# Optimization experiments

Hardware: AMD Instinct MI355X
Metric: run time of the kernel (lower is better)

Reference implementation:

```python
import jax, jax.numpy as jnp
import numpy as np

B_, T_, N_, C_ = 8, 24, 207, 128      # batch, time (fixed 24), nodes (fixed 207), channels
RED = C_ // 2                          # reducted_size = 64 (Mamba d_model)
DIN = 2 * RED                          # Mamba d_inner (expand=2) = 128
DS, DCONV, DTR = 16, 4, 4              # d_state, d_conv, dt_rank = ceil(64/16)


def _ln(x, w, b, eps=1e-5):
    m = jnp.mean(x, -1, keepdims=True)
    v = jnp.mean((x - m) ** 2, -1, keepdims=True)
    return (x - m) * jax.lax.rsqrt(v + eps) * w + b


def _causal_conv(x, w, b):
    # depthwise causal conv along seq; x: (B,L,D), w: (D,K)
    K = w.shape[1]
    L = x.shape[1]
    xp = jnp.pad(x, ((0, 0), (K - 1, 0), (0, 0)))
    return sum(xp[:, k:k + L, :] * w[:, k] for k in range(K)) + b


def _mamba(h, inproj, conv_w, conv_b, xproj, dtw, dtb, Alog, Dp, outproj):
    # mamba_ssm Mamba(d_model=RED) forward, eval mode
    xz = h @ inproj                                        # (B,L,2*DIN)
    u, z = jnp.split(xz, 2, axis=-1)
    u = jax.nn.silu(_causal_conv(u, conv_w, conv_b))       # (B,L,DIN)
    xdbl = u @ xproj                                       # (B,L,DTR+2*DS)
    dt = jax.nn.softplus(xdbl[..., :DTR] @ dtw + dtb)      # (B,L,DIN)
    Bm = xdbl[..., DTR:DTR + DS]                           # (B,L,DS)
    Cm = xdbl[..., DTR + DS:]                              # (B,L,DS)
    A = -jnp.exp(Alog)                                     # (DIN,DS)

    def step(hs, inp):
        dt_t, B_t, C_t, u_t = inp                          # (B,DIN),(B,DS),(B,DS),(B,DIN)
        hs = hs * jnp.exp(dt_t[..., None] * A) + (dt_t * u_t)[..., None] * B_t[:, None, :]
        return hs, jnp.einsum('bdn,bn->bd', hs, C_t)

    h0 = jnp.zeros((u.shape[0], DIN, DS), u.dtype)
    xs = (dt.swapaxes(0, 1), Bm.swapaxes(0, 1), Cm.swapaxes(0, 1), u.swapaxes(0, 1))
    _, ys = jax.lax.scan(step, h0, xs)                     # (L,B,DIN)
    y = ys.swapaxes(0, 1) + u * Dp
    y = y * jax.nn.silu(z)
    return y @ outproj                                     # (B,L,RED)


def setup_inputs() -> dict:
    key = jax.random.key(0)
    ks = iter(jax.random.split(key, 64))

    def rn(shape, s):
        return jax.random.normal(next(ks), shape, jnp.float32) * s

    inp = {
        "x": jax.random.normal(next(ks), (B_, T_, N_, C_), jnp.float32),
        "qk": jax.random.normal(next(ks), (B_, T_, N_, C_), jnp.float32),
        "in_ln_w": jnp.ones(2 * C_), "in_ln_b": jnp.zeros(2 * C_),
        "in_w": rn((2 * C_, RED), 0.05), "in_b": jnp.zeros(RED),
        "ov_ln_w": jnp.ones(RED), "ov_ln_b": jnp.zeros(RED),
        "ov_w": rn((RED, C_), 0.05), "ov_b": jnp.zeros(C_),
        "o_ln_w": jnp.ones(C_), "o_ln_b": jnp.zeros(C_),
        "o_w": rn((C_, C_), 0.05), "o_b": jnp.zeros(C_),
    }
    for p in ("fw", "bw"):
        inp[p + "_inproj"] = rn((RED, 2 * DIN), 0.05)
        inp[p + "_conv_w"] = rn((DIN, DCONV), 0.2)
        inp[p + "_conv_b"] = jnp.zeros(DIN)
        inp[p + "_xproj"] = rn((DIN, DTR + 2 * DS), 0.05)
        inp[p + "_dtw"] = rn((DTR, DIN), 0.2)
        dt0 = jnp.exp(jax.random.uniform(next(ks), (DIN,)) * (np.log(0.1) - np.log(1e-3)) + np.log(1e-3))
        inp[p + "_dtb"] = jnp.log(jnp.expm1(dt0))          # inverse softplus (mamba dt init)
        inp[p + "_Alog"] = jnp.log(jnp.broadcast_to(jnp.arange(1, DS + 1, dtype=jnp.float32), (DIN, DS)))
        inp[p + "_D"] = jnp.ones(DIN)
        inp[p + "_outproj"] = rn((DIN, RED), 0.05)
    return inp


def reference(x, qk, in_ln_w, in_ln_b, in_w, in_b,
              fw_inproj, fw_conv_w, fw_conv_b, fw_xproj, fw_dtw, fw_dtb, fw_Alog, fw_D, fw_outproj,
              bw_inproj, bw_conv_w, bw_conv_b, bw_xproj, bw_dtw, bw_dtb, bw_Alog, bw_D, bw_outproj,
              ov_ln_w, ov_ln_b, ov_w, ov_b, o_ln_w, o_ln_b, o_w, o_b):
    x_in = x
    h = jnp.concatenate([x, qk], -1).reshape(B_ * T_, N_, 2 * C_)   # 'b t n f -> (b t) n f'
    h = _ln(h, in_ln_w, in_ln_b) @ in_w + in_b                       # (B*T, N, RED)
    h_fw = _mamba(h, fw_inproj, fw_conv_w, fw_conv_b, fw_xproj, fw_dtw, fw_dtb, fw_Alog, fw_D, fw_outproj)
    h_bw = _mamba(h[:, ::-1], bw_inproj, bw_conv_w, bw_conv_b, bw_xproj, bw_dtw, bw_dtb, bw_Alog, bw_D, bw_outproj)[:, ::-1]
    h = h_fw + h_bw
    h = _ln(h, ov_ln_w, ov_ln_b) @ ov_w + ov_b                       # dropout: eval no-op
    h = h.reshape(B_, T_, N_, C_) + x_in                             # '(b t) n f -> b t n f' + residual
    return _ln(h, o_ln_w, o_ln_b) @ o_w + o_b
```

## Files before the change

### kernel.cpp

```cpp
#include <hip/hip_runtime.h>
#include <hip/hip_bf16.h>

#define B__ 8
#define T__ 24
#define N__ 207
#define C__ 128
#define BT_ 192
#define L__ 207
#define RED_ 64
#define DIN_ 128
#define DS_ 16
#define DTR_ 4
#define XD_ 36
#define NC_ 6
#define CHK_ 35
#define NROW_ 39744

#define P_OVLNW 0
#define P_OVLNB 64
#define P_OVB   128
#define P_OLNW  256
#define P_OLNB  384
#define P_OB    512
#define P_INB   640
#define P_LNW   704
#define P_LNB   960
#define P_TOT   1216

using bf16 = __hip_bfloat16;

typedef __attribute__((ext_vector_type(8))) short bf8v;
typedef __attribute__((ext_vector_type(4))) short s4v;
typedef __attribute__((ext_vector_type(4))) float f4v;

__device__ __forceinline__ float ldin(const void* __restrict__ p, int i, int md) {
    if (md) return ((const float*)p)[i];
    return __bfloat162float(((const bf16*)p)[i]);
}
__device__ __forceinline__ float ldbf(const bf16* __restrict__ p, int i) {
    return __bfloat162float(p[i]);
}

__device__ __forceinline__ short f2bf(float f) {
    unsigned u = __builtin_bit_cast(unsigned, f);
    unsigned r = (u + 0x7FFFu + ((u >> 16) & 1u)) >> 16;
    return (short)(unsigned short)r;
}
__device__ __forceinline__ float bfl(short h) {
    return __builtin_bit_cast(float, ((unsigned)(unsigned short)h) << 16);
}

__global__ void k0_detect(const void* __restrict__ lnw, int* __restrict__ mode,
                          int* __restrict__ geo) {
    unsigned short h0 = ((const unsigned short*)lnw)[0];
    *mode = (h0 == 0x3F80u) ? 0 : 1;
    *geo  = 1;
}

__global__ void probe_order_dict() {}
__global__ void probe_order_signature() {}

__global__ __launch_bounds__(256) void k_prep(
    const void* __restrict__ op_fw, const void* __restrict__ op_bw,
    const void* __restrict__ ovw, const void* __restrict__ ow,
    const void* __restrict__ ovlnw, const void* __restrict__ ovlnb,
    const void* __restrict__ ovb,
    const void* __restrict__ olnw, const void* __restrict__ olnb,
    const void* __restrict__ ob,
    const void* __restrict__ inw, const void* __restrict__ inb,
    const void* __restrict__ inlnw, const void* __restrict__ inlnb,
    const void* __restrict__ ipj_fw, const void* __restrict__ ipj_bw,
    const void* __restrict__ cw_fw, const void* __restrict__ cb_fw,
    const void* __restrict__ cw_bw, const void* __restrict__ cb_bw,
    const void* __restrict__ xp_fw, const void* __restrict__ xp_bw,
    const void* __restrict__ Alog_fw, const void* __restrict__ Alog_bw,
    short* __restrict__ w0t_hi, short* __restrict__ w0t_lo,
    short* __restrict__ w2t_hi, short* __restrict__ w2t_lo,
    short* __restrict__ w1t_hi, short* __restrict__ w1t_lo,
    short* __restrict__ ovwt_hi, short* __restrict__ ovwt_lo,
    short* __restrict__ owt_hi, short* __restrict__ owt_lo,
    short* __restrict__ w3t_hi, short* __restrict__ w3t_lo,
    float* __restrict__ cwt, float* __restrict__ cbt,
    float* __restrict__ pars, const int* __restrict__ mode,
    int* __restrict__ geo)
{
    const int md = *mode;
    const int stride = gridDim.x * blockDim.x;
    const int t0 = blockIdx.x * blockDim.x + threadIdx.x;
    for (int i = t0; i < 64*256; i += stride) {
        int c = i >> 8, k = i & 255;
        float wv = ldin(inw, k*64 + c, md);
        short h = f2bf(wv); w0t_hi[i] = h; w0t_lo[i] = f2bf(wv - bfl(h));
    }
    for (int i = t0; i < 2*256*64; i += stride) {
        int dir = i >> 14, c = (i >> 6) & 255, k = i & 63;
        const void* src = dir ? ipj_bw : ipj_fw;
        float wv = ldin(src, k*256 + c, md);
        short h = f2bf(wv); w2t_hi[i] = h; w2t_lo[i] = f2bf(wv - bfl(h));
    }
    for (int i = t0; i < 64*256; i += stride) {
        int c = i >> 8, k = i & 255;
        float wv = (k < 128) ? ldin(op_fw, k*64 + c, md)
                             : ldin(op_bw, (k-128)*64 + c, md);
        short h = f2bf(wv); w1t_hi[i] = h; w1t_lo[i] = f2bf(wv - bfl(h));
    }
    for (int i = t0; i < 128*64; i += stride) {
        int c = i >> 6, k = i & 63;
        float wv = ldin(ovw, k*128 + c, md);
        short h = f2bf(wv); ovwt_hi[i] = h; ovwt_lo[i] = f2bf(wv - bfl(h));
    }
    for (int i = t0; i < 128*128; i += stride) {
        int c = i >> 7, k = i & 127;
        float wv = ldin(ow, k*128 + c, md);
        short h = f2bf(wv); owt_hi[i] = h; owt_lo[i] = f2bf(wv - bfl(h));
    }
    for (int i = t0; i < 2*48*128; i += stride) {
        int dir = i / 6144, rem = i % 6144;
        int c = rem >> 7, k = rem & 127;
        float wv = (c < XD_) ? ldin(dir ? xp_bw : xp_fw, k*XD_ + c, md) : 0.f;
        short h = f2bf(wv); w3t_hi[i] = h; w3t_lo[i] = f2bf(wv - bfl(h));
    }
    for (int i = t0; i < 2*4*128; i += stride) {
        int dir = i >> 9, k = (i >> 7) & 3, d = i & 127;
        cwt[i] = ldin(dir ? cw_bw : cw_fw, d*4 + k, md);
    }
    for (int i = t0; i < 2*128; i += stride) {
        int dir = i >> 7, d = i & 127;
        cbt[i] = ldin(dir ? cb_bw : cb_fw, d, md);
    }
    for (int i = t0; i < 2*DIN_*DS_; i += stride) {
        int dir = i >> 11, rem = i & 2047;
        int d = rem >> 4, s = rem & 15;
        const void* Al = dir ? Alog_bw : Alog_fw;
        float A  = -__expf(ldin(Al, d*DS_ + s, md));
        float A0 = -__expf(ldin(Al, d*DS_ + 0, md));
        float tgt = (float)(s + 1) * A0;
        float tol = 1e-4f * fabsf(tgt) + 1e-6f;
        if (fabsf(A - tgt) > tol) atomicAnd(geo, 0);
    }
    for (int i = t0; i < P_TOT; i += stride) {
        float v;
        if      (i < 64)   v = ldin(ovlnw, i,        md);
        else if (i < 128)  v = ldin(ovlnb, i-64,     md);
        else if (i < 256)  v = ldin(ovb,   i-128,    md);
        else if (i < 384)  v = ldin(olnw,  i-256,    md);
        else if (i < 512)  v = ldin(olnb,  i-384,    md);
        else if (i < 640)  v = ldin(ob,    i-512,    md);
        else if (i < 704)  v = ldin(inb,   i-640,    md);
        else if (i < 960)  v = ldin(inlnw, i-704,    md);
        else               v = ldin(inlnb, i-960,    md);
        pars[i] = v;
    }
}

__global__ __launch_bounds__(64) void k12_mfma(
    const void* __restrict__ x, const void* __restrict__ qk,
    const short* __restrict__ w0t_hi, const short* __restrict__ w0t_lo,
    const short* __restrict__ w2t_hi, const short* __restrict__ w2t_lo,
    const float* __restrict__ pars,
    bf16* __restrict__ uraw, bf16* __restrict__ zbuf,
    const int* __restrict__ mode)
{
    const int md  = *mode;
    const int l   = threadIdx.x;
    const int lg  = l >> 4;
    const int lc  = l & 15;
    const int wrow = blockIdx.x * 16;
    const int dir  = blockIdx.y >> 1;
    const int nh   = blockIdx.y & 1;
    const int r = wrow + lc;

    __shared__ __align__(16) short t0h[16][136];
    __shared__ __align__(16) short t0l[16][136];
    __shared__ __align__(16) short hlds[16][80];

    const f4v zero = {0.f, 0.f, 0.f, 0.f};

    float s = 0.f, ss = 0.f;
    if (md) {
        const float* sp = ((lg < 2) ? (const float*)x : (const float*)qk)
                          + (size_t)r * C__ + (lg & 1) * 64;
#pragma unroll
        for (int t = 0; t < 16; ++t) {
            float4 v = *reinterpret_cast<const float4*>(sp + 4*t);
            s  += v.x + v.y + v.z + v.w;
            ss += v.x*v.x + v.y*v.y + v.z*v.z + v.w*v.w;
        }
    } else {
        const short* sp = ((lg < 2) ? (const short*)x : (const short*)qk)
                          + (size_t)r * C__ + (lg & 1) * 64;
#pragma unroll
        for (int t = 0; t < 8; ++t) {
            bf8v v = *reinterpret_cast<const bf8v*>(sp + 8*t);
#pragma unroll
            for (int e = 0; e < 8; ++e) { float f = bfl(v[e]); s += f; ss += f*f; }
        }
    }
    s  += __shfl_xor(s, 16, 64);  ss += __shfl_xor(ss, 16, 64);
    s  += __shfl_xor(s, 32, 64);  ss += __shfl_xor(ss, 32, 64);
    const float mean = s * (1.f/256.f);
    const float rs   = rsqrtf(ss * (1.f/256.f) - mean*mean + 1e-5f);

    f4v acc1[4];
#pragma unroll
    for (int nt = 0; nt < 4; ++nt) acc1[nt] = zero;

#pragma unroll
    for (int p = 0; p < 2; ++p) {
        const int hb = lg * 32;
        const int gcb = p * 128 + hb;
        if (md) {
            const float* sp = (p ? (const float*)qk : (const float*)x)
                              + (size_t)r * C__ + hb;
#pragma unroll
            for (int t = 0; t < 8; ++t) {
                float4 v = *reinterpret_cast<const float4*>(sp + 4*t);
                float vv[4] = {v.x, v.y, v.z, v.w};
                s4v hi, lo;
#pragma unroll
                for (int e = 0; e < 4; ++e) {
                    int gc = gcb + 4*t + e;
                    float a = (vv[e] - mean) * rs * pars[P_LNW + gc] + pars[P_LNB + gc];
                    short h = f2bf(a); hi[e] = h; lo[e] = f2bf(a - bfl(h));
                }
                *reinterpret_cast<s4v*>(&t0h[lc][hb + 4*t]) = hi;
                *reinterpret_cast<s4v*>(&t0l[lc][hb + 4*t]) = lo;
            }
        } else {
            const short* sp = (p ? (const short*)qk : (const short*)x)
                              + (size_t)r * C__ + hb;
#pragma unroll
            for (int t = 0; t < 4; ++t) {
                bf8v v = *reinterpret_cast<const bf8v*>(sp + 8*t);
#pragma unroll
                for (int hh = 0; hh < 2; ++hh) {
                    s4v hi, lo;
#pragma unroll
                    for (int e = 0; e < 4; ++e) {
                        int gc = gcb + 8*t + 4*hh + e;
                        float a = (bfl(v[4*hh+e]) - mean) * rs * pars[P_LNW + gc] + pars[P_LNB + gc];
                        short h = f2bf(a); hi[e] = h; lo[e] = f2bf(a - bfl(h));
                    }
                    *reinterpret_cast<s4v*>(&t0h[lc][hb + 8*t + 4*hh]) = hi;
                    *reinterpret_cast<s4v*>(&t0l[lc][hb + 8*t + 4*hh]) = lo;
                }
            }
        }
        __syncthreads();
#pragma unroll
        for (int kk = 0; kk < 4; ++kk) {
            bf8v ah = *reinterpret_cast<const bf8v*>(&t0h[lc][kk*32 + lg*8]);
            bf8v al = *reinterpret_cast<const bf8v*>(&t0l[lc][kk*32 + lg*8]);
#pragma unroll
            for (int nt = 0; nt < 4; ++nt) {
                const int bo = (nt*16 + lc)*256 + p*128 + kk*32 + lg*8;
                bf8v bh = *reinterpret_cast<const bf8v*>(w0t_hi + bo);
                bf8v bl = *reinterpret_cast<const bf8v*>(w0t_lo + bo);
                acc1[nt] = __builtin_amdgcn_mfma_f32_16x16x32_bf16(ah, bl, acc1[nt], 0, 0, 0);
                acc1[nt] = __builtin_amdgcn_mfma_f32_16x16x32_bf16(al, bh, acc1[nt], 0, 0, 0);
                acc1[nt] = __builtin_amdgcn_mfma_f32_16x16x32_bf16(ah, bh, acc1[nt], 0, 0, 0);
            }
        }
        __syncthreads();
    }

#pragma unroll
    for (int nt = 0; nt < 4; ++nt)
#pragma unroll
        for (int j = 0; j < 4; ++j)
            hlds[lg*4 + j][nt*16 + lc] = f2bf(acc1[nt][j] + pars[P_INB + nt*16 + lc]);
    __syncthreads();

    bf8v ha0 = *reinterpret_cast<const bf8v*>(&hlds[lc][lg*8]);
    bf8v ha1 = *reinterpret_cast<const bf8v*>(&hlds[lc][32 + lg*8]);

    const int g0 = wrow + lg*4;
    const int qg = g0 / 207, ng0 = g0 - qg * 207;

    f4v acc2[8];
#pragma unroll
    for (int nt = 0; nt < 8; ++nt) acc2[nt] = zero;
#pragma unroll
    for (int nt = 0; nt < 8; ++nt) {
        const int ntg = nh*8 + nt;
        const int co = dir*16384 + (ntg*16 + lc)*64;
        bf8v bh0 = *reinterpret_cast<const bf8v*>(w2t_hi + co + lg*8);
        bf8v bl0 = *reinterpret_cast<const bf8v*>(w2t_lo + co + lg*8);
        bf8v bh1 = *reinterpret_cast<const bf8v*>(w2t_hi + co + 32 + lg*8);
        bf8v bl1 = *reinterpret_cast<const bf8v*>(w2t_lo + co + 32 + lg*8);
        acc2[nt] = __builtin_amdgcn_mfma_f32_16x16x32_bf16(ha0, bl0, acc2[nt], 0, 0, 0);
        acc2[nt] = __builtin_amdgcn_mfma_f32_16x16x32_bf16(ha0, bh0, acc2[nt], 0, 0, 0);
        acc2[nt] = __builtin_amdgcn_mfma_f32_16x16x32_bf16(ha1, bl1, acc2[nt], 0, 0, 0);
        acc2[nt] = __builtin_amdgcn_mfma_f32_16x16x32_bf16(ha1, bh1, acc2[nt], 0, 0, 0);
    }
    bf16* __restrict__ dst = nh ? zbuf : uraw;
#pragma unroll
    for (int j = 0; j < 4; ++j) {
        int ng = ng0 + j, qq = qg;
        if (ng >= 207) { ng -= 207; ++qq; }
        const int ro = dir ? ((192 + qq)*207 + (206 - ng)) : (qq*207 + ng);
#pragma unroll
        for (int nt = 0; nt < 8; ++nt) {
            const int c = nt*16 + lc;
            dst[(size_t)ro*DIN_ + c] = __float2bfloat16(acc2[nt][j]);
        }
    }
}

__global__ __launch_bounds__(64) void k34_mfma(
    const bf16* __restrict__ uraw,
    const float* __restrict__ cwt, const float* __restrict__ cbt,
    const short* __restrict__ w3t_hi, const short* __restrict__ w3t_lo,
    bf16* __restrict__ ubuf, float* __restrict__ xdbl)
{
    const int l   = threadIdx.x;
    const int lg  = l >> 4;
    const int lc  = l & 15;
    const int wrow = blockIdx.x * 16;
    const int dir  = wrow / NROW_;
    const int r    = wrow + lc;
    const int m    = (r - dir * NROW_) % 207;

    __shared__ __align__(16) short uhh[16][136];
    __shared__ __align__(16) short ull[16][136];

    const float* __restrict__ cw = cwt + dir * 512;
    const float* __restrict__ cb = cbt + dir * 128;
    const int c0 = lg * 32;

#pragma unroll
    for (int t = 0; t < 4; ++t) {
        const int cc = c0 + t*8;
        float s[8];
#pragma unroll
        for (int e = 0; e < 8; ++e) s[e] = cb[cc + e];
#pragma unroll
        for (int k = 0; k < 3; ++k) {
            if (m - 3 + k >= 0) {
                bf8v v = *reinterpret_cast<const bf8v*>(
                    (const short*)uraw + (size_t)(r - 3 + k)*DIN_ + cc);
#pragma unroll
                for (int e = 0; e < 8; ++e) s[e] += bfl(v[e]) * cw[k*128 + cc + e];
            }
        }
        {
            bf8v v = *reinterpret_cast<const bf8v*>(
                (const short*)uraw + (size_t)r*DIN_ + cc);
#pragma unroll
            for (int e = 0; e < 8; ++e) s[e] += bfl(v[e]) * cw[3*128 + cc + e];
        }
        s4v h0, h1, l0, l1;
        bf8v uo;
#pragma unroll
        for (int e = 0; e < 8; ++e) {
            float u = s[e] / (1.f + __expf(-s[e]));
            short h = f2bf(u);
            short lo = f2bf(u - bfl(h));
            uo[e] = h;
            if (e < 4) { h0[e] = h; l0[e] = lo; }
            else       { h1[e-4] = h; l1[e-4] = lo; }
        }
        *reinterpret_cast<s4v*>(&uhh[lc][cc])     = h0;
        *reinterpret_cast<s4v*>(&uhh[lc][cc + 4]) = h1;
        *reinterpret_cast<s4v*>(&ull[lc][cc])     = l0;
        *reinterpret_cast<s4v*>(&ull[lc][cc + 4]) = l1;
        *reinterpret_cast<bf8v*>((short*)ubuf + (size_t)r*DIN_ + cc) = uo;
    }
    __syncthreads();

    const f4v zero = {0.f, 0.f, 0.f, 0.f};
    f4v acc[3];
#pragma unroll
    for (int nt = 0; nt < 3; ++nt) acc[nt] = zero;
    const int wb = dir * 6144;
#pragma unroll
    for (int kk = 0; kk < 4; ++kk) {
        bf8v ah = *reinterpret_cast<const bf8v*>(&uhh[lc][kk*32 + lg*8]);
        bf8v al = *reinterpret_cast<const bf8v*>(&ull[lc][kk*32 + lg*8]);
#pragma unroll
        for (int nt = 0; nt < 3; ++nt) {
            const int bo = wb + (nt*16 + lc)*128 + kk*32 + lg*8;
            bf8v bh = *reinterpret_cast<const bf8v*>(w3t_hi + bo);
            bf8v bl = *reinterpret_cast<const bf8v*>(w3t_lo + bo);
            acc[nt] = __builtin_amdgcn_mfma_f32_16x16x32_bf16(ah, bl, acc[nt], 0, 0, 0);
            acc[nt] = __builtin_amdgcn_mfma_f32_16x16x32_bf16(al, bh, acc[nt], 0, 0, 0);
            acc[nt] = __builtin_amdgcn_mfma_f32_16x16x32_bf16(ah, bh, acc[nt], 0, 0, 0);
        }
    }
#pragma unroll
    for (int nt = 0; nt < 3; ++nt) {
        const int c = nt*16 + lc;
        if (c < XD_) {
#pragma unroll
            for (int j = 0; j < 4; ++j)
                xdbl[(size_t)(wrow + lg*4 + j)*XD_ + c] = acc[nt][j];
        }
    }
}

__global__ __launch_bounds__(128) void k5a_local(
    const float* __restrict__ xdbl,
    const bf16* __restrict__ ubuf,
    float* __restrict__ h_end, float* __restrict__ sumdt,
    const void* __restrict__ dtw_fw, const void* __restrict__ dtb_fw,
    const void* __restrict__ Alog_fw,
    const void* __restrict__ dtw_bw, const void* __restrict__ dtb_bw,
    const void* __restrict__ Alog_bw,
    const int* __restrict__ mode, const int* __restrict__ geo)
{
    const int md = *mode;
    const int c = blockIdx.x, q = blockIdx.y, dir = blockIdx.z;
    const int d = threadIdx.x;
    const void* __restrict__ dtw  = dir ? dtw_bw  : dtw_fw;
    const void* __restrict__ dtbp = dir ? dtb_bw  : dtb_fw;
    const void* __restrict__ Alog = dir ? Alog_bw : Alog_fw;
    const float w0 = ldin(dtw, 0*DIN_ + d, md), w1 = ldin(dtw, 1*DIN_ + d, md);
    const float w2 = ldin(dtw, 2*DIN_ + d, md), w3 = ldin(dtw, 3*DIN_ + d, md);
    const float dtb = ldin(dtbp, d, md);
    float st[DS_];
#pragma unroll
    for (int s = 0; s < DS_; ++s) st[s] = 0.f;
    float sdt = 0.f;
    const int seq = dir*BT_ + q;
    const int m0 = c * CHK_;
    if (*geo) {
        const float A0 = -__expf(ldin(Alog, d*DS_ + 0, md));
        for (int m = m0; m < m0 + CHK_; ++m) {
            const float* __restrict__ xd = xdbl + (seq*L__ + m)*XD_;
            float4 xt = *reinterpret_cast<const float4*>(xd);
            float dtp = xt.x*w0 + xt.y*w1 + xt.z*w2 + xt.w*w3 + dtb;
            float dt = (dtp > 15.f) ? dtp : __logf(1.f + __expf(dtp));
            sdt += dt;
            float u = ldbf(ubuf, (seq*L__ + m)*DIN_ + d);
            float du = dt * u;
            float bb[DS_];
#pragma unroll
            for (int t = 0; t < 4; ++t) {
                float4 v = *reinterpret_cast<const float4*>(xd + DTR_ + 4*t);
                bb[4*t] = v.x; bb[4*t+1] = v.y; bb[4*t+2] = v.z; bb[4*t+3] = v.w;
            }
            float e1 = __expf(dt * A0);
            float pw = 1.f;
#pragma unroll
            for (int s = 0; s < DS_; ++s) {
                pw *= e1;
                st[s] = st[s]*pw + du*bb[s];
            }
        }
    } else {
        float A[DS_];
#pragma unroll
        for (int s = 0; s < DS_; ++s) A[s] = -__expf(ldin(Alog, d*DS_ + s, md));
        for (int m = m0; m < m0 + CHK_; ++m) {
            const float* __restrict__ xd = xdbl + (seq*L__ + m)*XD_;
            float4 xt = *reinterpret_cast<const float4*>(xd);
            float dtp = xt.x*w0 + xt.y*w1 + xt.z*w2 + xt.w*w3 + dtb;
            float dt = (dtp > 15.f) ? dtp : log1pf(__expf(dtp));
            sdt += dt;
            float u = ldbf(ubuf, (seq*L__ + m)*DIN_ + d);
            float du = dt * u;
            float bb[DS_];
#pragma unroll
            for (int t = 0; t < 4; ++t) {
                float4 v = *reinterpret_cast<const float4*>(xd + DTR_ + 4*t);
                bb[4*t] = v.x; bb[4*t+1] = v.y; bb[4*t+2] = v.z; bb[4*t+3] = v.w;
            }
#pragma unroll
            for (int s = 0; s < DS_; ++s)
                st[s] = st[s]*__expf(dt*A[s]) + du*bb[s];
        }
    }
    float* __restrict__ he = h_end + (size_t)(seq*5 + c)*(DIN_*DS_) + d*DS_;
#pragma unroll
    for (int t = 0; t < 4; ++t) {
        float4 v; v.x = st[4*t]; v.y = st[4*t+1]; v.z = st[4*t+2]; v.w = st[4*t+3];
        *reinterpret_cast<float4*>(he + 4*t) = v;
    }
    sumdt[(seq*5 + c)*DIN_ + d] = sdt;
}

__global__ __launch_bounds__(128) void k5c_scan(
    const float* __restrict__ xdbl,
    const bf16* __restrict__ zbuf,
    bf16* __restrict__ ubuf,
    const float* __restrict__ h_end, const float* __restrict__ sumdt,
    const void* __restrict__ dtw_fw, const void* __restrict__ dtb_fw,
    const void* __restrict__ Alog_fw, const void* __restrict__ D_fw,
    const void* __restrict__ dtw_bw, const void* __restrict__ dtb_bw,
    const void* __restrict__ Alog_bw, const void* __restrict__ D_bw,
    const int* __restrict__ mode, const int* __restrict__ geo)
{
    const int md = *mode;
    const int c = blockIdx.x, q = blockIdx.y, dir = blockIdx.z;
    const int d = threadIdx.x;
    const void* __restrict__ dtw  = dir ? dtw_bw  : dtw_fw;
    const void* __restrict__ dtbp = dir ? dtb_bw  : dtb_fw;
    const void* __restrict__ Alog = dir ? Alog_bw : Alog_fw;
    const void* __restrict__ Dp   = dir ? D_bw    : D_fw;
    const float w0 = ldin(dtw, 0*DIN_ + d, md), w1 = ldin(dtw, 1*DIN_ + d, md);
    const float w2 = ldin(dtw, 2*DIN_ + d, md), w3 = ldin(dtw, 3*DIN_ + d, md);
    const float dtb = ldin(dtbp, d, md), Dv = ldin(Dp, d, md);
    const int seq = dir*BT_ + q;
    const int m0 = c * CHK_;
    const int m1 = (m0 + CHK_ < L__) ? (m0 + CHK_) : L__;

    float st[DS_];
#pragma unroll
    for (int s = 0; s < DS_; ++s) st[s] = 0.f;

    if (*geo) {
        const float A0 = -__expf(ldin(Alog, d*DS_ + 0, md));
        for (int j = 0; j < c; ++j) {
            float sd = sumdt[(seq*5 + j)*DIN_ + d];
            const float* __restrict__ he = h_end + (size_t)(seq*5 + j)*(DIN_*DS_) + d*DS_;
            float hv[DS_];
#pragma unroll
            for (int t = 0; t < 4; ++t) {
                float4 v = *reinterpret_cast<const float4*>(he + 4*t);
                hv[4*t] = v.x; hv[4*t+1] = v.y; hv[4*t+2] = v.z; hv[4*t+3] = v.w;
            }
            float e1 = __expf(A0 * sd);
            float pw = 1.f;
#pragma unroll
            for (int s = 0; s < DS_; ++s) {
                pw *= e1;
                st[s] = st[s]*pw + hv[s];
            }
        }
        for (int m = m0; m < m1; ++m) {
            const float* __restrict__ xd = xdbl + (seq*L__ + m)*XD_;
            float4 xt = *reinterpret_cast<const float4*>(xd);
            float dtp = xt.x*w0 + xt.y*w1 + xt.z*w2 + xt.w*w3 + dtb;
            float dt = (dtp > 15.f) ? dtp : __logf(1.f + __expf(dtp));
            const int uidx = (seq*L__ + m)*DIN_ + d;
            float u = ldbf(ubuf, uidx);
            float du = dt * u;
            float bb[DS_], cc[DS_];
#pragma unroll
            for (int t = 0; t < 4; ++t) {
                float4 v = *reinterpret_cast<const float4*>(xd + DTR_ + 4*t);
                bb[4*t] = v.x; bb[4*t+1] = v.y; bb[4*t+2] = v.z; bb[4*t+3] = v.w;
                float4 w = *reinterpret_cast<const float4*>(xd + DTR_ + DS_ + 4*t);
                cc[4*t] = w.x; cc[4*t+1] = w.y; cc[4*t+2] = w.z; cc[4*t+3] = w.w;
            }
            float e1 = __expf(dt * A0);
            float pw = 1.f;
            float y = 0.f;
#pragma unroll
            for (int s = 0; s < DS_; ++s) {
                pw *= e1;
                st[s] = st[s]*pw + du*bb[s];
                y += st[s]*cc[s];
            }
            y += u * Dv;
            float z = ldbf(zbuf, uidx);
            y *= z / (1.f + __expf(-z));
            ubuf[uidx] = __float2bfloat16(y);
        }
    } else {
        float A[DS_];
#pragma unroll
        for (int s = 0; s < DS_; ++s) A[s] = -__expf(ldin(Alog, d*DS_ + s, md));
        for (int j = 0; j < c; ++j) {
            float sd = sumdt[(seq*5 + j)*DIN_ + d];
            const float* __restrict__ he = h_end + (size_t)(seq*5 + j)*(DIN_*DS_) + d*DS_;
            float hv[DS_];
#pragma unroll
            for (int t = 0; t < 4; ++t) {
                float4 v = *reinterpret_cast<const float4*>(he + 4*t);
                hv[4*t] = v.x; hv[4*t+1] = v.y; hv[4*t+2] = v.z; hv[4*t+3] = v.w;
            }
#pragma unroll
            for (int s = 0; s < DS_; ++s)
                st[s] = st[s]*__expf(A[s]*sd) + hv[s];
        }
        for (int m = m0; m < m1; ++m) {
            const float* __restrict__ xd = xdbl + (seq*L__ + m)*XD_;
            float4 xt = *reinterpret_cast<const float4*>(xd);
            float dtp = xt.x*w0 + xt.y*w1 + xt.z*w2 + xt.w*w3 + dtb;
            float dt = (dtp > 15.f) ? dtp : log1pf(__expf(dtp));
            const int uidx = (seq*L__ + m)*DIN_ + d;
            float u = ldbf(ubuf, uidx);
            float du = dt * u;
            float bb[DS_], cc[DS_];
#pragma unroll
            for (int t = 0; t < 4; ++t) {
                float4 v = *reinterpret_cast<const float4*>(xd + DTR_ + 4*t);
                bb[4*t] = v.x; bb[4*t+1] = v.y; bb[4*t+2] = v.z; bb[4*t+3] = v.w;
                float4 w = *reinterpret_cast<const float4*>(xd + DTR_ + DS_ + 4*t);
                cc[4*t] = w.x; cc[4*t+1] = w.y; cc[4*t+2] = w.z; cc[4*t+3] = w.w;
            }
            float y = 0.f;
#pragma unroll
            for (int s = 0; s < DS_; ++s) {
                st[s] = st[s]*__expf(dt*A[s]) + du*bb[s];
                y += st[s]*cc[s];
            }
            y += u * Dv;
            float z = ldbf(zbuf, uidx);
            y *= z / (1.f + __expf(-z));
            ubuf[uidx] = __float2bfloat16(y);
        }
    }
}

__global__ __launch_bounds__(64) void k6_mfma(
    const bf16* __restrict__ ubuf,
    const short* __restrict__ w1t_hi, const short* __restrict__ w1t_lo,
    const short* __restrict__ ovwt_hi, const short* __restrict__ ovwt_lo,
    const short* __restrict__ owt_hi, const short* __restrict__ owt_lo,
    const float* __restrict__ pars,
    const void* __restrict__ x, void* __restrict__ out,
    const int* __restrict__ mode)
{
    const int md  = *mode;
    const int l   = threadIdx.x;
    const int lg  = l >> 4;
    const int lc  = l & 15;
    const int wrow = blockIdx.x * 16;

    __shared__ __align__(16) short t1h[16][72];
    __shared__ __align__(16) short t1l[16][72];
    __shared__ __align__(16) short t2h[16][136];
    __shared__ __align__(16) short t2l[16][136];

    const f4v zero = {0.f, 0.f, 0.f, 0.f};

    const int ra = wrow + lc;
    const int qa = ra / 207, na = ra - qa * 207;
    const short* yfp = (const short*)ubuf + ra * 128 + lg * 8;
    const short* ybp = (const short*)ubuf + ((192 + qa) * 207 + (206 - na)) * 128 + lg * 8;

    f4v acc[4];
#pragma unroll
    for (int nt = 0; nt < 4; ++nt) acc[nt] = zero;

#pragma unroll
    for (int ks = 0; ks < 8; ++ks) {
        const short* ap = (ks < 4) ? (yfp + ks * 32) : (ybp + (ks - 4) * 32);
        bf8v a = *reinterpret_cast<const bf8v*>(ap);
#pragma unroll
        for (int nt = 0; nt < 4; ++nt) {
            const int bo = (nt * 16 + lc) * 256 + ks * 32 + lg * 8;
            bf8v bh = *reinterpret_cast<const bf8v*>(w1t_hi + bo);
            bf8v bl = *reinterpret_cast<const bf8v*>(w1t_lo + bo);
            acc[nt] = __builtin_amdgcn_mfma_f32_16x16x32_bf16(a, bl, acc[nt], 0, 0, 0);
            acc[nt] = __builtin_amdgcn_mfma_f32_16x16x32_bf16(a, bh, acc[nt], 0, 0, 0);
        }
    }

    {
        float sv[8];
#pragma unroll
        for (int i = 0; i < 8; ++i) sv[i] = 0.f;
#pragma unroll
        for (int nt = 0; nt < 4; ++nt)
#pragma unroll
            for (int j = 0; j < 4; ++j) { float v = acc[nt][j]; sv[j] += v; sv[4+j] += v*v; }
#pragma unroll
        for (int off = 8; off >= 1; off >>= 1)
#pragma unroll
            for (int i = 0; i < 8; ++i) sv[i] += __shfl_xor(sv[i], off, 64);
#pragma unroll
        for (int j = 0; j < 4; ++j) {
            float mean = sv[j] * (1.f/64.f);
            float var  = sv[4+j] * (1.f/64.f) - mean*mean;
            float rs   = rsqrtf(var + 1e-5f);
#pragma unroll
            for (int nt = 0; nt < 4; ++nt) {
                int c = nt*16 + lc;
                float t1 = (acc[nt][j] - mean) * rs * pars[c] + pars[64 + c];
                short h = f2bf(t1);
                t1h[lg*4+j][c] = h;
                t1l[lg*4+j][c] = f2bf(t1 - bfl(h));
            }
        }
    }
    __syncthreads();

    f4v acc2[8];
#pragma unroll
    for (int nt = 0; nt < 8; ++nt) acc2[nt] = zero;
#pragma unroll
    for (int ks = 0; ks < 2; ++ks) {
        bf8v a  = *reinterpret_cast<const bf8v*>(&t1h[lc][ks*32 + lg*8]);
        bf8v al = *reinterpret_cast<const bf8v*>(&t1l[lc][ks*32 + lg*8]);
#pragma unroll
        for (int nt = 0; nt < 8; ++nt) {
            const int bo = (nt*16 + lc) * 64 + ks*32 + lg*8;
            bf8v bh = *reinterpret_cast<const bf8v*>(ovwt_hi + bo);
            bf8v bl = *reinterpret_cast<const bf8v*>(ovwt_lo + bo);
            acc2[nt] = __builtin_amdgcn_mfma_f32_16x16x32_bf16(a,  bh, acc2[nt], 0, 0, 0);
            acc2[nt] = __builtin_amdgcn_mfma_f32_16x16x32_bf16(a,  bl, acc2[nt], 0, 0, 0);
            acc2[nt] = __builtin_amdgcn_mfma_f32_16x16x32_bf16(al, bh, acc2[nt], 0, 0, 0);
        }
    }

    const int rc = wrow + lg*4;
#pragma unroll
    for (int nt = 0; nt < 8; ++nt)
#pragma unroll
        for (int j = 0; j < 4; ++j) acc2[nt][j] += pars[128 + nt*16 + lc];
    if (md) {
        const float* xf = (const float*)x;
#pragma unroll
        for (int nt = 0; nt < 8; ++nt)
#pragma unroll
            for (int j = 0; j < 4; ++j)
                acc2[nt][j] += xf[(rc + j)*128 + nt*16 + lc];
    } else {
        const bf16* xb = (const bf16*)x;
#pragma unroll
        for (int nt = 0; nt < 8; ++nt)
#pragma unroll
            for (int j = 0; j < 4; ++j)
                acc2[nt][j] += ldbf(xb, (rc + j)*128 + nt*16 + lc);
    }

    {
        float sv[8];
#pragma unroll
        for (int i = 0; i < 8; ++i) sv[i] = 0.f;
#pragma unroll
        for (int nt = 0; nt < 8; ++nt)
#pragma unroll
            for (int j = 0; j < 4; ++j) { float v = acc2[nt][j]; sv[j] += v; sv[4+j] += v*v; }
#pragma unroll
        for (int off = 8; off >= 1; off >>= 1)
#pragma unroll
            for (int i = 0; i < 8; ++i) sv[i] += __shfl_xor(sv[i], off, 64);
#pragma unroll
        for (int j = 0; j < 4; ++j) {
            float mean = sv[j] * (1.f/128.f);
            float var  = sv[4+j] * (1.f/128.f) - mean*mean;
            float rs   = rsqrtf(var + 1e-5f);
#pragma unroll
            for (int nt = 0; nt < 8; ++nt) {
                int c = nt*16 + lc;
                float t2 = (acc2[nt][j] - mean) * rs * pars[256 + c] + pars[384 + c];
                short h = f2bf(t2);
                t2h[lg*4+j][c] = h;
                t2l[lg*4+j][c] = f2bf(t2 - bfl(h));
            }
        }
    }
    __syncthreads();

    f4v acc3[8];
#pragma unroll
    for (int nt = 0; nt < 8; ++nt) acc3[nt] = zero;
#pragma unroll
    for (int ks = 0; ks < 4; ++ks) {
        bf8v a  = *reinterpret_cast<const bf8v*>(&t2h[lc][ks*32 + lg*8]);
        bf8v al = *reinterpret_cast<const bf8v*>(&t2l[lc][ks*32 + lg*8]);
#pragma unroll
        for (int nt = 0; nt < 8; ++nt) {
            const int bo = (nt*16 + lc) * 128 + ks*32 + lg*8;
            bf8v bh = *reinterpret_cast<const bf8v*>(owt_hi + bo);
            bf8v bl = *reinterpret_cast<const bf8v*>(owt_lo + bo);
            acc3[nt] = __builtin_amdgcn_mfma_f32_16x16x32_bf16(a,  bh, acc3[nt], 0, 0, 0);
            acc3[nt] = __builtin_amdgcn_mfma_f32_16x16x32_bf16(a,  bl, acc3[nt], 0, 0, 0);
            acc3[nt] = __builtin_amdgcn_mfma_f32_16x16x32_bf16(al, bh, acc3[nt], 0, 0, 0);
        }
    }
    if (md) {
        float* of = (float*)out;
#pragma unroll
        for (int nt = 0; nt < 8; ++nt)
#pragma unroll
            for (int j = 0; j < 4; ++j) {
                int c = nt*16 + lc;
                of[(rc + j)*128 + c] = acc3[nt][j] + pars[512 + c];
            }
    } else {
        bf16* ob_ = (bf16*)out;
#pragma unroll
        for (int nt = 0; nt < 8; ++nt)
#pragma unroll
            for (int j = 0; j < 4; ++j) {
                int c = nt*16 + lc;
                ob_[(rc + j)*128 + c] = __float2bfloat16(acc3[nt][j] + pars[512 + c]);
            }
    }
}

extern "C" void kernel_launch(void* const* d_in, const int* in_sizes, int n_in,
                              void* d_out, int out_size, void* d_ws, size_t ws_size,
                              hipStream_t stream)
{
    const bool sig = (n_in > 6) && (in_sizes[6] == 16384);

    const void *x, *qk, *inlnw, *inlnb, *inw, *inb;
    const void *ovlnw, *ovlnb, *ovw, *ovb, *olnw, *olnb, *ow, *ob;
    const void *fw_inproj, *fw_convw, *fw_convb, *fw_xproj, *fw_dtw, *fw_dtb,
               *fw_Alog, *fw_D, *fw_outproj;
    const void *bw_inproj, *bw_convw, *bw_convb, *bw_xproj, *bw_dtw, *bw_dtb,
               *bw_Alog, *bw_D, *bw_outproj;

    x = d_in[0]; qk = d_in[1]; inlnw = d_in[2]; inlnb = d_in[3];
    inw = d_in[4]; inb = d_in[5];
    if (!sig) {
        ovlnw = d_in[6];  ovlnb = d_in[7];  ovw = d_in[8];  ovb = d_in[9];
        olnw  = d_in[10]; olnb  = d_in[11]; ow  = d_in[12]; ob  = d_in[13];
        fw_inproj = d_in[14]; fw_convw = d_in[15]; fw_convb = d_in[16];
        fw_xproj = d_in[17]; fw_dtw = d_in[18]; fw_dtb = d_in[19];
        fw_Alog = d_in[20]; fw_D = d_in[21]; fw_outproj = d_in[22];
        bw_inproj = d_in[23]; bw_convw = d_in[24]; bw_convb = d_in[25];
        bw_xproj = d_in[26]; bw_dtw = d_in[27]; bw_dtb = d_in[28];
        bw_Alog = d_in[29]; bw_D = d_in[30]; bw_outproj = d_in[31];
    } else {
        fw_inproj = d_in[6];  fw_convw = d_in[7];  fw_convb = d_in[8];
        fw_xproj = d_in[9];  fw_dtw = d_in[10]; fw_dtb = d_in[11];
        fw_Alog = d_in[12]; fw_D = d_in[13]; fw_outproj = d_in[14];
        bw_inproj = d_in[15]; bw_convw = d_in[16]; bw_convb = d_in[17];
        bw_xproj = d_in[18]; bw_dtw = d_in[19]; bw_dtb = d_in[20];
        bw_Alog = d_in[21]; bw_D = d_in[22]; bw_outproj = d_in[23];
        ovlnw = d_in[24]; ovlnb = d_in[25]; ovw = d_in[26]; ovb = d_in[27];
        olnw  = d_in[28]; olnb  = d_in[29]; ow  = d_in[30]; ob  = d_in[31];
    }

    char* ws = (char*)d_ws;
    int*   mode = (int*)(ws);
    int*   geo  = (int*)(ws + 8);
    float* sumdt = (float*)(ws + 16);
    short* w0t_hi  = (short*)(ws + 983056);
    short* w0t_lo  = (short*)(ws + 1015824);
    short* w2t_hi  = (short*)(ws + 1048592);
    short* w2t_lo  = (short*)(ws + 1114128);
    bf16*  uraw = (bf16*)(ws + 5087248);
    float* h_end = (float*)(ws + 5087248);
    bf16*  zbuf = (bf16*)(ws + 25436176);
    bf16*  ubuf = (bf16*)(ws + 45785104);
    float* xdbl = (float*)(ws + 66134032);
    short* w1t_hi  = (short*)(ws + 77580304);
    short* w1t_lo  = (short*)(ws + 77613072);
    short* ovwt_hi = (short*)(ws + 77645840);
    short* ovwt_lo = (short*)(ws + 77662224);
    short* owt_hi  = (short*)(ws + 77678608);
    short* owt_lo  = (short*)(ws + 77711376);
    float* pars    = (float*)(ws + 77744144);
    short* w3t_hi  = (short*)(ws + 77749008);
    short* w3t_lo  = (short*)(ws + 77773584);
    float* cwt     = (float*)(ws + 77798160);
    float* cbt     = (float*)(ws + 77802256);

    if (sig) probe_order_signature<<<1, 64, 0, stream>>>();
    else     probe_order_dict<<<1, 64, 0, stream>>>();

    k0_detect<<<1, 1, 0, stream>>>(inlnw, mode, geo);
    k_prep<<<40, 256, 0, stream>>>(
        fw_outproj, bw_outproj, ovw, ow,
        ovlnw, ovlnb, ovb, olnw, olnb, ob,
        inw, inb, inlnw, inlnb, fw_inproj, bw_inproj,
        fw_convw, fw_convb, bw_convw, bw_convb, fw_xproj, bw_xproj,
        fw_Alog, bw_Alog,
        w0t_hi, w0t_lo, w2t_hi, w2t_lo,
        w1t_hi, w1t_lo, ovwt_hi, ovwt_lo, owt_hi, owt_lo,
        w3t_hi, w3t_lo, cwt, cbt, pars, mode, geo);
    k12_mfma<<<dim3(2484, 4), 64, 0, stream>>>(
        x, qk, w0t_hi, w0t_lo, w2t_hi, w2t_lo, pars, uraw, zbuf, mode);
    k34_mfma<<<dim3(4968), 64, 0, stream>>>(
        uraw, cwt, cbt, w3t_hi, w3t_lo, ubuf, xdbl);
    k5a_local<<<dim3(NC_-1, BT_, 2), 128, 0, stream>>>(
        xdbl, ubuf, h_end, sumdt,
        fw_dtw, fw_dtb, fw_Alog,
        bw_dtw, bw_dtb, bw_Alog, mode, geo);
    k5c_scan<<<dim3(NC_, BT_, 2), 128, 0, stream>>>(
        xdbl, zbuf, ubuf, h_end, sumdt,
        fw_dtw, fw_dtb, fw_Alog, fw_D,
        bw_dtw, bw_dtb, bw_Alog, bw_D, mode, geo);
    k6_mfma<<<dim3(2484), 64, 0, stream>>>(
        ubuf, w1t_hi, w1t_lo, ovwt_hi, ovwt_lo, owt_hi, owt_lo, pars,
        x, d_out, mode);
}
```

Before: 475.1 us.

## Split fused LN+in_proj kernel to avoid recomputing first GEMM per output quarter

The fused kernel ran on a 2484x4 grid, so each of the four y-blocks recomputed the layernorm and the 256->64 input projection for the same rows. The change moves that stage into its own kernel that runs once per row tile and writes h in bf16 to a workspace buffer aliased with xdbl. A second kernel then reads h and does the 64->256 in_proj for both directions. This removes the fourfold redundant LN and GEMM work, including the repeated reads of x and qk, at the cost of an extra launch and a global round trip for h.

```diff
diff --git a/kernel.cpp b/kernel.cpp
--- a/kernel.cpp
+++ b/kernel.cpp
@@ -153,26 +153,21 @@
     }
 }
 
-__global__ __launch_bounds__(64) void k12_mfma(
+__global__ __launch_bounds__(64) void k1_mfma(
     const void* __restrict__ x, const void* __restrict__ qk,
     const short* __restrict__ w0t_hi, const short* __restrict__ w0t_lo,
-    const short* __restrict__ w2t_hi, const short* __restrict__ w2t_lo,
     const float* __restrict__ pars,
-    bf16* __restrict__ uraw, bf16* __restrict__ zbuf,
-    const int* __restrict__ mode)
+    bf16* __restrict__ hbuf, const int* __restrict__ mode)
 {
     const int md  = *mode;
     const int l   = threadIdx.x;
     const int lg  = l >> 4;
     const int lc  = l & 15;
     const int wrow = blockIdx.x * 16;
-    const int dir  = blockIdx.y >> 1;
-    const int nh   = blockIdx.y & 1;
     const int r = wrow + lc;
 
     __shared__ __align__(16) short t0h[16][136];
     __shared__ __align__(16) short t0l[16][136];
-    __shared__ __align__(16) short hlds[16][80];
 
     const f4v zero = {0.f, 0.f, 0.f, 0.f};
 
@@ -264,16 +259,32 @@
         __syncthreads();
     }
 
+    short* hp = (short*)hbuf;
 #pragma unroll
     for (int nt = 0; nt < 4; ++nt)
 #pragma unroll
         for (int j = 0; j < 4; ++j)
-            hlds[lg*4 + j][nt*16 + lc] = f2bf(acc1[nt][j] + pars[P_INB + nt*16 + lc]);
-    __syncthreads();
-
-    bf8v ha0 = *reinterpret_cast<const bf8v*>(&hlds[lc][lg*8]);
-    bf8v ha1 = *reinterpret_cast<const bf8v*>(&hlds[lc][32 + lg*8]);
-
+            hp[(size_t)(wrow + lg*4 + j)*RED_ + nt*16 + lc] =
+                f2bf(acc1[nt][j] + pars[P_INB + nt*16 + lc]);
+}
+
+__global__ __launch_bounds__(64) void k2_mfma(
+    const bf16* __restrict__ hbuf,
+    const short* __restrict__ w2t_hi, const short* __restrict__ w2t_lo,
+    bf16* __restrict__ uraw, bf16* __restrict__ zbuf)
+{
+    const int l   = threadIdx.x;
+    const int lg  = l >> 4;
+    const int lc  = l & 15;
+    const int wrow = blockIdx.x * 16;
+    const int dir  = blockIdx.y >> 1;
+    const int nh   = blockIdx.y & 1;
+
+    const short* hp = (const short*)hbuf + (size_t)(wrow + lc) * RED_;
+    bf8v ha0 = *reinterpret_cast<const bf8v*>(hp + lg*8);
+    bf8v ha1 = *reinterpret_cast<const bf8v*>(hp + 32 + lg*8);
+
+    const f4v zero = {0.f, 0.f, 0.f, 0.f};
     const int g0 = wrow + lg*4;
     const int qg = g0 / 207, ng0 = g0 - qg * 207;
 
@@ -832,6 +843,7 @@
     bf16*  zbuf = (bf16*)(ws + 25436176);
     bf16*  ubuf = (bf16*)(ws + 45785104);
     float* xdbl = (float*)(ws + 66134032);
+    bf16*  hbuf = (bf16*)(ws + 66134032);
     short* w1t_hi  = (short*)(ws + 77580304);
     short* w1t_lo  = (short*)(ws + 77613072);
     short* ovwt_hi = (short*)(ws + 77645840);
@@ -857,8 +869,10 @@
         w0t_hi, w0t_lo, w2t_hi, w2t_lo,
         w1t_hi, w1t_lo, ovwt_hi, ovwt_lo, owt_hi, owt_lo,
         w3t_hi, w3t_lo, cwt, cbt, pars, mode, geo);
-    k12_mfma<<<dim3(2484, 4), 64, 0, stream>>>(
-        x, qk, w0t_hi, w0t_lo, w2t_hi, w2t_lo, pars, uraw, zbuf, mode);
+    k1_mfma<<<dim3(2484), 64, 0, stream>>>(
+        x, qk, w0t_hi, w0t_lo, pars, hbuf, mode);
+    k2_mfma<<<dim3(2484, 4), 64, 0, stream>>>(
+        hbuf, w2t_hi, w2t_lo, uraw, zbuf);
     k34_mfma<<<dim3(4968), 64, 0, stream>>>(
         uraw, cwt, cbt, w3t_hi, w3t_lo, ubuf, xdbl);
     k5a_local<<<dim3(NC_-1, BT_, 2), 128, 0, stream>>>(
```

After: 396.3 us. 16.6% less time.
